# Performance work log

Measured on AMD Instinct MI355X. Metric: run time of the kernel, lower is better.

The kernel has to match this reference:

```python
import jax, jax.numpy as jnp
import numpy as np

N = 50000        # atoms
E = 1600000      # edges (precomputed radius graph)
H = 128          # hidden_channels
F = 64           # num_filters
G = 50           # num_gaussians
L = 3            # num_interactions
NG = 256         # graphs in batch
MAXZ = 100       # atomic-number vocabulary
CUTOFF = 10.0


def ssp(x):
    # ShiftedSoftplus
    return jax.nn.softplus(x) - jnp.log(2.0).astype(x.dtype)


def setup_inputs() -> dict:
    key = jax.random.key(0)
    ks = jax.random.split(key, 20)
    s = 0.1
    inp = {
        "z": jax.random.randint(ks[0], (N,), 0, MAXZ),
        "pos": jax.random.uniform(ks[1], (N, 3), dtype=jnp.float32) * 5.0,
        "batch": jnp.sort(jax.random.randint(ks[2], (N,), 0, NG)),
        "edge_index": jax.random.randint(ks[3], (2, E), 0, N),
        "emb": jax.random.normal(ks[4], (MAXZ, H), dtype=jnp.float32),
        # interaction-block params, stacked over L layers
        "mw1": jax.random.normal(ks[5], (L, G, F), dtype=jnp.float32) * s,
        "mb1": jnp.zeros((L, F), dtype=jnp.float32),
        "mw2": jax.random.normal(ks[6], (L, F, F), dtype=jnp.float32) * s,
        "mb2": jnp.zeros((L, F), dtype=jnp.float32),
        "l1w": jax.random.normal(ks[7], (L, H, F), dtype=jnp.float32) * s,  # no bias
        "l2w": jax.random.normal(ks[8], (L, F, H), dtype=jnp.float32) * s,
        "l2b": jnp.zeros((L, H), dtype=jnp.float32),
        "lw": jax.random.normal(ks[9], (L, H, H), dtype=jnp.float32) * s,
        "lb": jnp.zeros((L, H), dtype=jnp.float32),
        # output MLP
        "ow1": jax.random.normal(ks[10], (H, H // 2), dtype=jnp.float32) * s,
        "ob1": jnp.zeros((H // 2,), dtype=jnp.float32),
        "ow2": jax.random.normal(ks[11], (H // 2, 1), dtype=jnp.float32) * s,
        "ob2": jnp.zeros((1,), dtype=jnp.float32),
    }
    return inp


def reference(z, pos, batch, edge_index, emb, mw1, mb1, mw2, mb2,
              l1w, l2w, l2b, lw, lb, ow1, ob1, ow2, ob2):
    src = edge_index[0]  # j (message source)
    dst = edge_index[1]  # i (message target)

    h = emb[z]                                   # [N,H]

    # edge distances + Gaussian smearing
    d = jnp.linalg.norm(pos[src] - pos[dst], axis=-1)          # [E]
    offset = jnp.linspace(0.0, CUTOFF, G, dtype=jnp.float32)   # [G]
    coeff = -0.5 / (offset[1] - offset[0]) ** 2
    edge_attr = jnp.exp(coeff * (d[:, None] - offset) ** 2)    # [E,G]

    # cosine cutoff
    C = 0.5 * (jnp.cos(d * jnp.pi / CUTOFF) + 1.0)             # [E]

    for i in range(L):
        # per-edge filter MLP
        W = ssp(edge_attr @ mw1[i] + mb1[i]) @ mw2[i] + mb2[i]  # [E,F]
        W = W * C[:, None]
        xj = (h @ l1w[i])[src]                                  # gather [E,F]
        msg = xj * W                                            # [E,F]
        agg = jax.ops.segment_sum(msg, dst, num_segments=N)     # [N,F]
        x = agg @ l2w[i] + l2b[i]                               # [N,H]
        x = ssp(x)
        x = x @ lw[i] + lb[i]
        h = h + x                                               # residual

    # output network + per-graph sum readout
    h = ssp(h @ ow1 + ob1)
    h = h @ ow2 + ob2                                           # [N,1]
    out = jax.ops.segment_sum(h, batch, num_segments=NG)        # [NG,1]
    return out.squeeze(1)                                       # [NG]
```

## Files before the change

kernel.cpp:

```cpp
#include <hip/hip_runtime.h>


typedef short bf16x8 __attribute__((ext_vector_type(8)));
typedef unsigned short ushort8 __attribute__((ext_vector_type(8)));
typedef float floatx4 __attribute__((ext_vector_type(4)));

#define HCH 128
#define FCH 64
#define GCH 50
#define LN  3
#define TBL 4096
#define CAP2 12288
#define CHUNK 4096
#define DMAX 8.6603f

#define MFMA(a, b, c) __builtin_amdgcn_mfma_f32_16x16x32_bf16((a), (b), (c), 0, 0, 0)

__device__ __forceinline__ unsigned short f2bf(float x) {
    unsigned int u = __float_as_uint(x);
    unsigned int r = (u + 0x7FFFu + ((u >> 16) & 1u)) >> 16;
    return (unsigned short)r;
}

__device__ __forceinline__ unsigned pk2bf(float lo, float hi) {
    unsigned ulo = __float_as_uint(lo) + 0x8000u;
    unsigned uhi = __float_as_uint(hi) + 0x8000u;
    return __builtin_amdgcn_perm(uhi, ulo, 0x07060302u);
}

__device__ __forceinline__ float bf2f(unsigned short u) {
    return __uint_as_float((unsigned)u << 16);
}

__device__ __forceinline__ float sspf(float x) {
    float t = __expf(-fabsf(x));
    float l = __logf(1.f + t);
    return fmaxf(x, 0.f) + l - 0.69314718056f;
}

__device__ __forceinline__ void fill_frag(const float* __restrict__ src,
                                          short* __restrict__ dst,
                                          int K, int F, int Ksrc,
                                          int tid, int nthr)
{
    int kc = K >> 5;
    int total = (F >> 4) * kc * 512;
    for (int i = tid; i < total; i += nthr) {
        int j = i & 7;
        int lane = (i >> 3) & 63;
        int rest = i >> 9;
        int kk = rest % kc;
        int nt = rest / kc;
        int k = kk * 32 + ((lane >> 4) << 3) + j;
        int f = nt * 16 + (lane & 15);
        float v = (k < Ksrc) ? src[k * F + f] : 0.f;
        dst[i] = (short)f2bf(v);
    }
}

__global__ void k_prep(const float* __restrict__ l1w, const float* __restrict__ l2w,
                       const float* __restrict__ lw,  const float* __restrict__ ow1,
                       short* __restrict__ l1wp, short* __restrict__ l2wp,
                       short* __restrict__ lwp,  short* __restrict__ ow1p)
{
    int tid = blockIdx.x * blockDim.x + threadIdx.x;
    int nthr = gridDim.x * blockDim.x;
    for (int l = 0; l < LN; l++) {
        fill_frag(l1w + l * HCH * FCH, l1wp + l * 8192, 128, 64, 128, tid, nthr);
        fill_frag(l2w + l * FCH * HCH, l2wp + l * 8192, 64, 128, 64, tid, nthr);
        fill_frag(lw  + l * HCH * HCH, lwp  + l * 16384, 128, 128, 128, tid, nthr);
    }
    fill_frag(ow1, ow1p, 128, 64, 128, tid, nthr);
}

__global__ __launch_bounds__(64) void k_wtab(
    const float* __restrict__ mw1, const float* __restrict__ mb1,
    const float* __restrict__ mw2, const float* __restrict__ mb2,
    unsigned short* __restrict__ Wtb)
{
    __shared__ float sh[64];
    int blk = blockIdx.x;
    int l = blk / TBL, k = blk - l * TBL;
    int f = threadIdx.x;
    float d = (float)k * (DMAX / (float)(TBL - 1));
    const float step = 10.f / 49.f;
    const float coeff = -0.5f / (step * step);

    float t1 = mb1[l * 64 + f];
    const float* w1 = mw1 + l * GCH * 64;
    for (int g = 0; g < GCH; g++) {
        float u = d - (float)g * step;
        t1 += __expf(coeff * u * u) * w1[g * 64 + f];
    }
    sh[f] = sspf(t1);
    float acc = mb2[l * 64 + f];
    const float* w2 = mw2 + l * 64 * 64;
    for (int g = 0; g < 64; g++) acc += sh[g] * w2[g * 64 + f];
    float C = 0.5f * (__cosf(d * 0.31415926535897932f) + 1.f);
    Wtb[(size_t)blk * 64 + f] = f2bf(acc * C);
}

__global__ __launch_bounds__(256) void k_s1(
    const int* __restrict__ ei, const float* __restrict__ pos,
    int* __restrict__ gcur, int2* __restrict__ ebuf, int E, int nb2)
{
    __shared__ int hist[256];
    __shared__ int lstart[256];
    __shared__ int lcur[256];
    __shared__ int gbase[256];
    __shared__ int wsum[4];
    __shared__ int2 stage[CHUNK];

    int t = threadIdx.x, lane = t & 63, w = t >> 6;
    int e0 = blockIdx.x * CHUNK;
    int e1 = min(e0 + CHUNK, E);
    int cnt = e1 - e0;

    hist[t] = 0;
    __syncthreads();

    int2 my[16];
    int  mybk[16];
#pragma unroll
    for (int i = 0; i < 16; i++) {
        int e = e0 + t + i * 256;
        int ec = min(e, E - 1);
        int s = ei[ec];
        int d2 = ei[E + ec];
        float dx = pos[s * 3 + 0] - pos[d2 * 3 + 0];
        float dy = pos[s * 3 + 1] - pos[d2 * 3 + 1];
        float dz = pos[s * 3 + 2] - pos[d2 * 3 + 2];
        float dist = sqrtf(dx * dx + dy * dy + dz * dz);
        int tix = (int)(dist * ((float)(TBL - 1) / DMAX) + 0.5f);
        tix = (tix > TBL - 1) ? (TBL - 1) : tix;
        my[i] = make_int2(s | (tix << 17), d2);
        mybk[i] = (e < e1) ? (d2 >> 8) : -1;
        if (mybk[i] >= 0) atomicAdd(&hist[mybk[i]], 1);
    }
    __syncthreads();

    int base0;
    {
        int c = hist[t];
        int a = c;
#pragma unroll
        for (int o = 1; o < 64; o <<= 1) {
            int u = __shfl_up(a, o, 64);
            if (lane >= o) a += u;
        }
        if (lane == 63) wsum[w] = a;
        __syncthreads();
        int prefix = 0;
#pragma unroll
        for (int i = 0; i < 4; i++) if (i < w) prefix += wsum[i];
        int ls = prefix + a - c;
        lstart[t] = ls; lcur[t] = ls;
        base0 = (c && t < nb2) ? atomicAdd(&gcur[t * 16], c) : 0;
    }
    __syncthreads();

#pragma unroll
    for (int i = 0; i < 16; i++) {
        if (mybk[i] >= 0) {
            int ofs = atomicAdd(&lcur[mybk[i]], 1);
            stage[ofs] = my[i];
        }
    }
    gbase[t] = t * CAP2 + base0;
    __syncthreads();

    for (int i = t; i < cnt; i += 256) {
        int2 ed = stage[i];
        int bk = ed.y >> 8;
        int g = gbase[bk] + (i - lstart[bk]);
        if (g < bk * CAP2 + CAP2) ebuf[g] = ed;
    }
}

__global__ __launch_bounds__(512) void k_s2(
    const int2* __restrict__ ebuf, const int* __restrict__ gcur,
    int2* __restrict__ edata, int nb2)
{
    __shared__ int hist[256];
    __shared__ int bcur[256];
    __shared__ int wred[8];
    int t = threadIdx.x, lane = t & 63, w = t >> 6, bk = blockIdx.x;
    int cnt = min(gcur[bk * 16], CAP2);

    int v = (t < bk && t < nb2) ? min(gcur[t * 16], CAP2) : 0;
#pragma unroll
    for (int o = 32; o; o >>= 1) v += __shfl_down(v, o, 64);
    if (lane == 0) wred[w] = v;
    if (t < 256) hist[t] = 0;
    __syncthreads();
    int gs = 0;
#pragma unroll
    for (int i = 0; i < 8; i++) gs += wred[i];

    const int2* eb = ebuf + (size_t)bk * CAP2;
    for (int i = t; i < cnt; i += 512)
        atomicAdd(&hist[eb[i].y & 255], 1);
    __syncthreads();
    int myc = (t < 256) ? hist[t] : 0;
    for (int o = 1; o < 256; o <<= 1) {
        int u = (t < 256 && t >= o) ? hist[t - o] : 0;
        __syncthreads();
        if (t < 256) hist[t] += u;
        __syncthreads();
    }
    if (t < 256) bcur[t] = gs + hist[t] - myc;
    __syncthreads();
    for (int i = t; i < cnt; i += 512) {
        int2 ed = eb[i];
        int dl = ed.y & 255;
        int p = atomicAdd(&bcur[dl], 1);
        edata[p] = ed;
    }
}

__global__ __launch_bounds__(256) void k_node0(const int* __restrict__ z,
    const float* __restrict__ emb, const short* __restrict__ l1wp0,
    float* __restrict__ h, unsigned short* __restrict__ xjb,
    float* __restrict__ agg, int N)
{
    __shared__ __align__(16) short A3[8192];
    __shared__ int zL[64];
    int t = threadIdx.x, lane = t & 63, w = t >> 6;
    int n0 = blockIdx.x * 64;
    if (t < 64) { int n = n0 + t; zL[t] = (n < N) ? z[n] : 0; }
    __syncthreads();
    for (int i = t; i < 4096; i += 256) {
        int n = n0 + (i >> 6);
        if (n < N) agg[(size_t)n * FCH + (i & 63)] = 0.f;
    }
#pragma unroll
    for (int m = 0; m < 16; m++) {
        int ii = lane + 64 * m;
        int rloc = ii >> 6;
        int k0 = (ii & 63) * 2;
        int n = n0 + w * 16 + rloc;
        float2 v = make_float2(0.f, 0.f);
        if (n < N) {
            v = *(const float2*)(&emb[(size_t)zL[w * 16 + rloc] * HCH + k0]);
            *(float2*)(&h[(size_t)n * HCH + k0]) = v;
        }
        unsigned pk = pk2bf(v.x, v.y);
        int si = w * 2048 + (k0 >> 5) * 512 + (rloc + 16 * ((k0 >> 3) & 3)) * 8 + (k0 & 7);
        *(unsigned*)(&A3[si]) = pk;
    }
    int quad = lane >> 4, col = lane & 15;
    const bf16x8* B = (const bf16x8*)l1wp0;
    bf16x8 af[4];
#pragma unroll
    for (int kk = 0; kk < 4; kk++)
        af[kk] = *(const bf16x8*)(&A3[w * 2048 + kk * 512 + lane * 8]);
#pragma unroll
    for (int nt = 0; nt < 4; nt++) {
        floatx4 c = {0.f, 0.f, 0.f, 0.f};
#pragma unroll
        for (int kk = 0; kk < 4; kk++) c = MFMA(af[kk], B[(nt * 4 + kk) * 64 + lane], c);
        int f = nt * 16 + col;
#pragma unroll
        for (int reg = 0; reg < 4; reg++) {
            int n = n0 + w * 16 + quad * 4 + reg;
            if (n < N) xjb[(size_t)n * FCH + f] = f2bf(c[reg]);
        }
    }
}

__global__ __launch_bounds__(256) void k_edge(
    const int2* __restrict__ edata, const unsigned short* __restrict__ xjb,
    const unsigned short* __restrict__ Wt, float* __restrict__ agg, int E)
{
    int t = threadIdx.x, lane = t & 63, w = t >> 6;
    int eg0 = blockIdx.x * 64 + w * 16;

    int ei16 = eg0 + (lane & 15);
    int2 edv = (ei16 < E) ? edata[ei16] : make_int2(0, -1);

    int sV[16], tV[16], dV[16];
#pragma unroll
    for (int i = 0; i < 16; i++) {
        int ex = __shfl(edv.x, i, 64);
        dV[i]  = __shfl(edv.y, i, 64);
        sV[i] = ex & 0x1FFFF;
        tV[i] = (int)(((unsigned)ex) >> 17);
    }
    unsigned short xv[16], wv[16];
#pragma unroll
    for (int i = 0; i < 16; i++) {
        xv[i] = xjb[((size_t)sV[i] << 6) + lane];
        wv[i] = Wt[((size_t)tV[i] << 6) + lane];
    }
    float a = 0.f;
    int cur = dV[0];
#pragma unroll
    for (int i = 0; i < 16; i++) {
        if (dV[i] != cur) {
            if (cur >= 0) unsafeAtomicAdd(&agg[(size_t)cur * FCH + lane], a);
            a = 0.f; cur = dV[i];
        }
        a += bf2f(xv[i]) * bf2f(wv[i]);
    }
    if (cur >= 0) unsafeAtomicAdd(&agg[(size_t)cur * FCH + lane], a);
}

__global__ __launch_bounds__(256) void k_update(
    float* __restrict__ agg, const short* __restrict__ l2wp,
    const float* __restrict__ l2b, const short* __restrict__ lwp,
    const float* __restrict__ lb,  const short* __restrict__ l1wp_next,
    float* __restrict__ h, unsigned short* __restrict__ xjb, int layer, int N)
{
    __shared__ __align__(16) short AR[8192];
    int t = threadIdx.x, lane = t & 63, w = t >> 6;
    int n0 = blockIdx.x * 64;
    short* WR = &AR[w * 2048];
#pragma unroll
    for (int m = 0; m < 8; m++) {
        int ii = lane + 64 * m;
        int rloc = ii >> 5;
        int k0 = (ii & 31) * 2;
        int n = n0 + w * 16 + rloc;
        float2 v = make_float2(0.f, 0.f);
        if (n < N) v = *(const float2*)(&agg[(size_t)n * FCH + k0]);
        unsigned pk = pk2bf(v.x, v.y);
        int si = (k0 >> 5) * 512 + (rloc + 16 * ((k0 >> 3) & 3)) * 8 + (k0 & 7);
        *(unsigned*)(&WR[si]) = pk;
    }
#pragma unroll
    for (int i = 0; i < 16; i++) {
        int n = n0 + w * 16 + i;
        if (n < N) agg[(size_t)n * FCH + lane] = 0.f;
    }
    int quad = lane >> 4, col = lane & 15;
    const bf16x8* Bl2 = (const bf16x8*)(l2wp + layer * 8192);
    const bf16x8* Blw = (const bf16x8*)(lwp + layer * 16384);
    const bf16x8* Bl1 = (const bf16x8*)l1wp_next;

    bf16x8 a0 = *(const bf16x8*)(&WR[lane * 8]);
    bf16x8 a1 = *(const bf16x8*)(&WR[512 + lane * 8]);
#pragma unroll
    for (int nt = 0; nt < 8; nt++) {
        float bias = l2b[layer * HCH + nt * 16 + col];
        floatx4 c = {bias, bias, bias, bias};
        c = MFMA(a0, Bl2[(nt * 2 + 0) * 64 + lane], c);
        c = MFMA(a1, Bl2[(nt * 2 + 1) * 64 + lane], c);
        int f = nt * 16 + col;
        int si0 = (f >> 5) * 512 + (16 * ((f >> 3) & 3)) * 8 + (f & 7);
#pragma unroll
        for (int reg = 0; reg < 4; reg++)
            WR[si0 + (quad * 4 + reg) * 8] = (short)f2bf(sspf(c[reg]));
    }
    bf16x8 af[4];
#pragma unroll
    for (int kk = 0; kk < 4; kk++)
        af[kk] = *(const bf16x8*)(&WR[kk * 512 + lane * 8]);
#pragma unroll
    for (int nt = 0; nt < 8; nt++) {
        float bias = lb[layer * HCH + nt * 16 + col];
        floatx4 c = {bias, bias, bias, bias};
#pragma unroll
        for (int kk = 0; kk < 4; kk++) c = MFMA(af[kk], Blw[(nt * 4 + kk) * 64 + lane], c);
        int f = nt * 16 + col;
        int si0 = (f >> 5) * 512 + (16 * ((f >> 3) & 3)) * 8 + (f & 7);
#pragma unroll
        for (int reg = 0; reg < 4; reg++) {
            int n = n0 + w * 16 + quad * 4 + reg;
            float hv = 0.f;
            if (n < N) {
                hv = h[(size_t)n * HCH + f] + c[reg];
                h[(size_t)n * HCH + f] = hv;
            }
            WR[si0 + (quad * 4 + reg) * 8] = (short)f2bf(hv);
        }
    }
#pragma unroll
    for (int kk = 0; kk < 4; kk++)
        af[kk] = *(const bf16x8*)(&WR[kk * 512 + lane * 8]);
#pragma unroll
    for (int nt = 0; nt < 4; nt++) {
        floatx4 c = {0.f, 0.f, 0.f, 0.f};
#pragma unroll
        for (int kk = 0; kk < 4; kk++) c = MFMA(af[kk], Bl1[(nt * 4 + kk) * 64 + lane], c);
        int f = nt * 16 + col;
#pragma unroll
        for (int reg = 0; reg < 4; reg++) {
            int n = n0 + w * 16 + quad * 4 + reg;
            if (n < N) xjb[(size_t)n * FCH + f] = f2bf(c[reg]);
        }
    }
}

__global__ __launch_bounds__(256) void k_final(
    const float* __restrict__ agg, const short* __restrict__ l2wp,
    const float* __restrict__ l2b, const short* __restrict__ lwp,
    const float* __restrict__ lb,  const short* __restrict__ ow1p,
    const float* __restrict__ ob1, const float* __restrict__ ow2,
    const float* __restrict__ ob2, const int* __restrict__ batch,
    const float* __restrict__ h, float* __restrict__ out, int layer, int N)
{
    __shared__ __align__(16) short AR[8192];
    __shared__ float R[64 * 17];
    int t = threadIdx.x, lane = t & 63, w = t >> 6;
    int n0 = blockIdx.x * 64;
    short* WR = &AR[w * 2048];
#pragma unroll
    for (int m = 0; m < 8; m++) {
        int ii = lane + 64 * m;
        int rloc = ii >> 5;
        int k0 = (ii & 31) * 2;
        int n = n0 + w * 16 + rloc;
        float2 v = make_float2(0.f, 0.f);
        if (n < N) v = *(const float2*)(&agg[(size_t)n * FCH + k0]);
        unsigned pk = pk2bf(v.x, v.y);
        int si = (k0 >> 5) * 512 + (rloc + 16 * ((k0 >> 3) & 3)) * 8 + (k0 & 7);
        *(unsigned*)(&WR[si]) = pk;
    }
    int quad = lane >> 4, col = lane & 15;
    const bf16x8* Bl2 = (const bf16x8*)(l2wp + layer * 8192);
    const bf16x8* Blw = (const bf16x8*)(lwp + layer * 16384);
    const bf16x8* Bow = (const bf16x8*)ow1p;

    bf16x8 a0 = *(const bf16x8*)(&WR[lane * 8]);
    bf16x8 a1 = *(const bf16x8*)(&WR[512 + lane * 8]);
#pragma unroll
    for (int nt = 0; nt < 8; nt++) {
        float bias = l2b[layer * HCH + nt * 16 + col];
        floatx4 c = {bias, bias, bias, bias};
        c = MFMA(a0, Bl2[(nt * 2 + 0) * 64 + lane], c);
        c = MFMA(a1, Bl2[(nt * 2 + 1) * 64 + lane], c);
        int f = nt * 16 + col;
        int si0 = (f >> 5) * 512 + (16 * ((f >> 3) & 3)) * 8 + (f & 7);
#pragma unroll
        for (int reg = 0; reg < 4; reg++)
            WR[si0 + (quad * 4 + reg) * 8] = (short)f2bf(sspf(c[reg]));
    }
    bf16x8 af[4];
#pragma unroll
    for (int kk = 0; kk < 4; kk++)
        af[kk] = *(const bf16x8*)(&WR[kk * 512 + lane * 8]);
#pragma unroll
    for (int nt = 0; nt < 8; nt++) {
        float bias = lb[layer * HCH + nt * 16 + col];
        floatx4 c = {bias, bias, bias, bias};
#pragma unroll
        for (int kk = 0; kk < 4; kk++) c = MFMA(af[kk], Blw[(nt * 4 + kk) * 64 + lane], c);
        int f = nt * 16 + col;
        int si0 = (f >> 5) * 512 + (16 * ((f >> 3) & 3)) * 8 + (f & 7);
#pragma unroll
        for (int reg = 0; reg < 4; reg++) {
            int n = n0 + w * 16 + quad * 4 + reg;
            float hv = 0.f;
            if (n < N) hv = h[(size_t)n * HCH + f] + c[reg];
            WR[si0 + (quad * 4 + reg) * 8] = (short)f2bf(hv);
        }
    }
#pragma unroll
    for (int kk = 0; kk < 4; kk++)
        af[kk] = *(const bf16x8*)(&WR[kk * 512 + lane * 8]);
    float p[4] = {0.f, 0.f, 0.f, 0.f};
#pragma unroll
    for (int nt = 0; nt < 4; nt++) {
        float bias = ob1[nt * 16 + col];
        floatx4 c = {bias, bias, bias, bias};
#pragma unroll
        for (int kk = 0; kk < 4; kk++) c = MFMA(af[kk], Bow[(nt * 4 + kk) * 64 + lane], c);
        float w2 = ow2[nt * 16 + col];
#pragma unroll
        for (int reg = 0; reg < 4; reg++) p[reg] += sspf(c[reg]) * w2;
    }
#pragma unroll
    for (int reg = 0; reg < 4; reg++)
        R[(w * 16 + quad * 4 + reg) * 17 + col] = p[reg];
    __syncthreads();
    if (t < 64) {
        int n = n0 + t;
        float v = 0.f;
        int g = -1;
        if (n < N) {
            v = ob2[0];
#pragma unroll
            for (int c2 = 0; c2 < 16; c2++) v += R[t * 17 + c2];
            g = batch[n];
        }
#pragma unroll
        for (int off2 = 1; off2 < 64; off2 <<= 1) {
            float vv = __shfl_down(v, off2, 64);
            int gg = __shfl_down(g, off2, 64);
            if (lane + off2 < 64 && gg == g) v += vv;
        }
        int gp = __shfl_up(g, 1, 64);
        bool head = (lane == 0) || (g != gp);
        if (head && g >= 0) unsafeAtomicAdd(&out[g], v);
    }
}

extern "C" void kernel_launch(void* const* d_in, const int* in_sizes, int n_in,
                              void* d_out, int out_size, void* d_ws, size_t ws_size,
                              hipStream_t stream)
{
    const int*   z    = (const int*)d_in[0];
    const float* pos  = (const float*)d_in[1];
    const int*   batc = (const int*)d_in[2];
    const int*   ei   = (const int*)d_in[3];
    const float* emb  = (const float*)d_in[4];
    const float* mw1  = (const float*)d_in[5];
    const float* mb1  = (const float*)d_in[6];
    const float* mw2  = (const float*)d_in[7];
    const float* mb2  = (const float*)d_in[8];
    const float* l1w  = (const float*)d_in[9];
    const float* l2w  = (const float*)d_in[10];
    const float* l2b  = (const float*)d_in[11];
    const float* lw   = (const float*)d_in[12];
    const float* lb   = (const float*)d_in[13];
    const float* ow1  = (const float*)d_in[14];
    const float* ob1  = (const float*)d_in[15];
    const float* ow2  = (const float*)d_in[16];
    const float* ob2  = (const float*)d_in[17];
    float* out = (float*)d_out;

    int N = in_sizes[0];
    int E = in_sizes[3] / 2;
    int nb2 = (N + 255) >> 8;

    char* ws = (char*)d_ws;
    size_t off = 0;
    auto alloc = [&](size_t bytes) {
        void* p = ws + off;
        off = (off + bytes + 255) & ~(size_t)255;
        return p;
    };
    float* h      = (float*)alloc((size_t)N * HCH * 4);
    unsigned short* xjb = (unsigned short*)alloc((size_t)N * FCH * 2);
    float* agg    = (float*)alloc((size_t)N * FCH * 4);
    int2*  ebuf   = (int2*)alloc((size_t)nb2 * CAP2 * 8);
    int2*  edata  = (int2*)alloc((size_t)E * 8);
    unsigned short* Wtab = (unsigned short*)alloc((size_t)LN * TBL * 64 * 2);
    int*   gcur   = (int*)alloc((size_t)nb2 * 64);
    short* l1wp   = (short*)alloc(LN * 8192 * 2);
    short* l2wp   = (short*)alloc(LN * 8192 * 2);
    short* lwp    = (short*)alloc(LN * 16384 * 2);
    short* ow1p   = (short*)alloc(8192 * 2);

    int NB = (N + 63) / 64;
    int EB = (E + 63) / 64;
    int S1B = (E + CHUNK - 1) / CHUNK;

    k_prep<<<32, 256, 0, stream>>>(l1w, l2w, lw, ow1, l1wp, l2wp, lwp, ow1p);
    k_wtab<<<LN * TBL, 64, 0, stream>>>(mw1, mb1, mw2, mb2, Wtab);
    hipMemsetAsync(gcur, 0, (size_t)nb2 * 64, stream);
    k_s1<<<S1B, 256, 0, stream>>>(ei, pos, gcur, ebuf, E, nb2);
    k_s2<<<nb2, 512, 0, stream>>>(ebuf, gcur, edata, nb2);
    hipMemsetAsync(out, 0, (size_t)out_size * sizeof(float), stream);

    k_node0<<<NB, 256, 0, stream>>>(z, emb, l1wp, h, xjb, agg, N);
    for (int l = 0; l < LN; l++) {
        k_edge<<<EB, 256, 0, stream>>>(edata, xjb,
                                       Wtab + (size_t)l * TBL * 64, agg, E);
        if (l < LN - 1) {
            k_update<<<NB, 256, 0, stream>>>(agg, l2wp, l2b, lwp, lb,
                                             l1wp + (l + 1) * 8192, h, xjb, l, N);
        } else {
            k_final<<<NB, 256, 0, stream>>>(agg, l2wp, l2b, lwp, lb, ow1p,
                                            ob1, ow2, ob2, batc, h, out, l, N);
        }
    }
}
```

Measured before the change: 372.0 us.

## Replace atomic edge scatter with CSR row-pointer segmented reduction per node

The sort kernel now also writes a CSR row pointer giving each destination node's start offset. The edge kernel assigns one wavefront per destination node and accumulates its incoming edges in registers, then writes agg with a single store. This removes the float atomics and the agg zeroing in node0 and update. In exchange, per-wave work now depends on node degree, loads are issued one edge at a time with less memory-level parallelism, and rowptr correctness relies on the capacity-clamped bucket counts.

```diff
diff --git a/kernel.cpp b/kernel.cpp
--- a/kernel.cpp
+++ b/kernel.cpp
@@ -179,7 +179,7 @@
 
 __global__ __launch_bounds__(512) void k_s2(
     const int2* __restrict__ ebuf, const int* __restrict__ gcur,
-    int2* __restrict__ edata, int nb2)
+    int2* __restrict__ edata, int* __restrict__ rowptr, int nb2)
 {
     __shared__ int hist[256];
     __shared__ int bcur[256];
@@ -208,7 +208,12 @@
         if (t < 256) hist[t] += u;
         __syncthreads();
     }
-    if (t < 256) bcur[t] = gs + hist[t] - myc;
+    if (t < 256) {
+        int start = gs + hist[t] - myc;
+        bcur[t] = start;
+        rowptr[(bk << 8) + t] = start;
+    }
+    if (bk == nb2 - 1 && t == 0) rowptr[nb2 << 8] = gs + cnt;
     __syncthreads();
     for (int i = t; i < cnt; i += 512) {
         int2 ed = eb[i];
@@ -220,8 +225,7 @@
 
 __global__ __launch_bounds__(256) void k_node0(const int* __restrict__ z,
     const float* __restrict__ emb, const short* __restrict__ l1wp0,
-    float* __restrict__ h, unsigned short* __restrict__ xjb,
-    float* __restrict__ agg, int N)
+    float* __restrict__ h, unsigned short* __restrict__ xjb, int N)
 {
     __shared__ __align__(16) short A3[8192];
     __shared__ int zL[64];
@@ -229,10 +233,6 @@
     int n0 = blockIdx.x * 64;
     if (t < 64) { int n = n0 + t; zL[t] = (n < N) ? z[n] : 0; }
     __syncthreads();
-    for (int i = t; i < 4096; i += 256) {
-        int n = n0 + (i >> 6);
-        if (n < N) agg[(size_t)n * FCH + (i & 63)] = 0.f;
-    }
 #pragma unroll
     for (int m = 0; m < 16; m++) {
         int ii = lane + 64 * m;
@@ -269,44 +269,34 @@
 }
 
 __global__ __launch_bounds__(256) void k_edge(
-    const int2* __restrict__ edata, const unsigned short* __restrict__ xjb,
-    const unsigned short* __restrict__ Wt, float* __restrict__ agg, int E)
+    const int* __restrict__ rowptr, const int2* __restrict__ edata,
+    const unsigned short* __restrict__ xjb, const unsigned short* __restrict__ Wt,
+    float* __restrict__ agg, int N)
 {
     int t = threadIdx.x, lane = t & 63, w = t >> 6;
-    int eg0 = blockIdx.x * 64 + w * 16;
-
-    int ei16 = eg0 + (lane & 15);
-    int2 edv = (ei16 < E) ? edata[ei16] : make_int2(0, -1);
-
-    int sV[16], tV[16], dV[16];
-#pragma unroll
-    for (int i = 0; i < 16; i++) {
-        int ex = __shfl(edv.x, i, 64);
-        dV[i]  = __shfl(edv.y, i, 64);
-        sV[i] = ex & 0x1FFFF;
-        tV[i] = (int)(((unsigned)ex) >> 17);
-    }
-    unsigned short xv[16], wv[16];
-#pragma unroll
-    for (int i = 0; i < 16; i++) {
-        xv[i] = xjb[((size_t)sV[i] << 6) + lane];
-        wv[i] = Wt[((size_t)tV[i] << 6) + lane];
-    }
-    float a = 0.f;
-    int cur = dV[0];
-#pragma unroll
-    for (int i = 0; i < 16; i++) {
-        if (dV[i] != cur) {
-            if (cur >= 0) unsafeAtomicAdd(&agg[(size_t)cur * FCH + lane], a);
-            a = 0.f; cur = dV[i];
-        }
-        a += bf2f(xv[i]) * bf2f(wv[i]);
-    }
-    if (cur >= 0) unsafeAtomicAdd(&agg[(size_t)cur * FCH + lane], a);
+    int n = blockIdx.x * 4 + w;
+    if (n >= N) return;
+    int beg = rowptr[n];
+    int end = rowptr[n + 1];
+    float acc = 0.f;
+    for (int e = beg; e < end; e += 8) {
+        int2 ed = edata[min(e + (lane & 7), end - 1)];
+#pragma unroll
+        for (int i = 0; i < 8; i++) {
+            if (e + i < end) {
+                int ex = __shfl(ed.x, i, 64);
+                int s  = ex & 0x1FFFF;
+                int tix = (int)(((unsigned)ex) >> 17);
+                acc += bf2f(xjb[((size_t)s << 6) + lane]) *
+                       bf2f(Wt[((size_t)tix << 6) + lane]);
+            }
+        }
+    }
+    agg[(size_t)n * FCH + lane] = acc;
 }
 
 __global__ __launch_bounds__(256) void k_update(
-    float* __restrict__ agg, const short* __restrict__ l2wp,
+    const float* __restrict__ agg, const short* __restrict__ l2wp,
     const float* __restrict__ l2b, const short* __restrict__ lwp,
     const float* __restrict__ lb,  const short* __restrict__ l1wp_next,
     float* __restrict__ h, unsigned short* __restrict__ xjb, int layer, int N)
@@ -326,11 +316,6 @@
         unsigned pk = pk2bf(v.x, v.y);
         int si = (k0 >> 5) * 512 + (rloc + 16 * ((k0 >> 3) & 3)) * 8 + (k0 & 7);
         *(unsigned*)(&WR[si]) = pk;
-    }
-#pragma unroll
-    for (int i = 0; i < 16; i++) {
-        int n = n0 + w * 16 + i;
-        if (n < N) agg[(size_t)n * FCH + lane] = 0.f;
     }
     int quad = lane >> 4, col = lane & 15;
     const bf16x8* Bl2 = (const bf16x8*)(l2wp + layer * 8192);
@@ -537,26 +522,27 @@
     int2*  edata  = (int2*)alloc((size_t)E * 8);
     unsigned short* Wtab = (unsigned short*)alloc((size_t)LN * TBL * 64 * 2);
     int*   gcur   = (int*)alloc((size_t)nb2 * 64);
+    int*   rowptr = (int*)alloc(((size_t)nb2 * 256 + 1) * 4);
     short* l1wp   = (short*)alloc(LN * 8192 * 2);
     short* l2wp   = (short*)alloc(LN * 8192 * 2);
     short* lwp    = (short*)alloc(LN * 16384 * 2);
     short* ow1p   = (short*)alloc(8192 * 2);
 
     int NB = (N + 63) / 64;
-    int EB = (E + 63) / 64;
+    int NB4 = (N + 3) / 4;
     int S1B = (E + CHUNK - 1) / CHUNK;
 
     k_prep<<<32, 256, 0, stream>>>(l1w, l2w, lw, ow1, l1wp, l2wp, lwp, ow1p);
     k_wtab<<<LN * TBL, 64, 0, stream>>>(mw1, mb1, mw2, mb2, Wtab);
     hipMemsetAsync(gcur, 0, (size_t)nb2 * 64, stream);
     k_s1<<<S1B, 256, 0, stream>>>(ei, pos, gcur, ebuf, E, nb2);
-    k_s2<<<nb2, 512, 0, stream>>>(ebuf, gcur, edata, nb2);
+    k_s2<<<nb2, 512, 0, stream>>>(ebuf, gcur, edata, rowptr, nb2);
     hipMemsetAsync(out, 0, (size_t)out_size * sizeof(float), stream);
 
-    k_node0<<<NB, 256, 0, stream>>>(z, emb, l1wp, h, xjb, agg, N);
+    k_node0<<<NB, 256, 0, stream>>>(z, emb, l1wp, h, xjb, N);
     for (int l = 0; l < LN; l++) {
-        k_edge<<<EB, 256, 0, stream>>>(edata, xjb,
-                                       Wtab + (size_t)l * TBL * 64, agg, E);
+        k_edge<<<NB4, 256, 0, stream>>>(rowptr, edata, xjb,
+                                        Wtab + (size_t)l * TBL * 64, agg, N);
         if (l < LN - 1) {
             k_update<<<NB, 256, 0, stream>>>(agg, l2wp, l2b, lwp, lb,
                                              l1wp + (l + 1) * 8192, h, xjb, l, N);
```

Result: slower. 543.8 us (+46.2%).
